# Performance work log

Measured on AMD Instinct MI355X. Metric: run time of the kernel, lower is better.

Reference implementation:

```python
import jax, jax.numpy as jnp
import numpy as np

NC, ND = 100000, 100000
E, L = 500000, 100000
HID, OUT = 128, 64
NH, HD = 4, 32
NL = 2


def setup_inputs() -> dict:
    key = jax.random.key(0)
    ks = jax.random.split(key, 16)
    f = jnp.float32
    s_lin = 1.0 / np.sqrt(HID)
    s_rel = 1.0 / np.sqrt(HD)
    return {
        "emb_C": jax.random.normal(ks[0], (NC, HID), f) * 0.1,
        "emb_D": jax.random.normal(ks[1], (ND, HID), f) * 0.1,
        "kW": jax.random.normal(ks[2], (NL, 2, HID, HID), f) * s_lin,
        "kb": jnp.zeros((NL, 2, HID), f),
        "qW": jax.random.normal(ks[3], (NL, 2, HID, HID), f) * s_lin,
        "qb": jnp.zeros((NL, 2, HID), f),
        "vW": jax.random.normal(ks[4], (NL, 2, HID, HID), f) * s_lin,
        "vb": jnp.zeros((NL, 2, HID), f),
        "aW": jax.random.normal(ks[5], (NL, 2, HID, HID), f) * s_lin,
        "ab": jnp.zeros((NL, 2, HID), f),
        "skip": jnp.ones((NL, 2), f),
        "arel": jax.random.normal(ks[6], (NL, 2, NH, HD, HD), f) * s_rel,
        "mrel": jax.random.normal(ks[7], (NL, 2, NH, HD, HD), f) * s_rel,
        "prel": jnp.ones((NL, 2, NH), f),
        "outW": jax.random.normal(ks[8], (2, HID, OUT), f) * s_lin,
        "outb": jnp.zeros((2, OUT), f),
        # edge_index for (Compound -> Disease) and reverse (Disease -> Compound)
        "ei_cd": jnp.stack([jax.random.randint(ks[9], (E,), 0, NC),
                            jax.random.randint(ks[10], (E,), 0, ND)]).astype(jnp.int32),
        "ei_dc": jnp.stack([jax.random.randint(ks[11], (E,), 0, ND),
                            jax.random.randint(ks[12], (E,), 0, NC)]).astype(jnp.int32),
        # edge_label_index: (Compound, Disease) pairs to score
        "eli": jnp.stack([jax.random.randint(ks[13], (L,), 0, NC),
                          jax.random.randint(ks[14], (L,), 0, ND)]).astype(jnp.int32),
    }


def _seg_softmax(a, seg, n):
    # numerically stable softmax over edges grouped by destination node
    amax = jax.ops.segment_max(a, seg, num_segments=n)
    amax = jnp.where(jnp.isfinite(amax), amax, 0.0)
    ex = jnp.exp(a - amax[seg])
    den = jax.ops.segment_sum(ex, seg, num_segments=n)
    return ex / (den[seg] + 1e-16)


def _hgt_layer(xs, p, ei_cd, ei_dc):
    kW, kb, qW, qb, vW, vb, aW, ab, skip, arel, mrel, prel = p
    # per-node-type K/Q/V projections, reshaped to [N, heads, head_dim]
    k = [(xs[t] @ kW[t] + kb[t]).reshape(-1, NH, HD) for t in range(2)]
    q = [(xs[t] @ qW[t] + qb[t]).reshape(-1, NH, HD) for t in range(2)]
    v = [(xs[t] @ vW[t] + vb[t]).reshape(-1, NH, HD) for t in range(2)]
    outs = [jnp.zeros_like(k[0]), jnp.zeros_like(k[1])]
    rels = [(0, 1, ei_cd), (1, 0, ei_dc)]  # (src_type, dst_type, edge_index)
    for r, (s, d, ei) in enumerate(rels):
        # relation-specific transforms applied per source node (as in PyG HGTConv)
        krel = jnp.einsum('nhd,hde->nhe', k[s], arel[r])
        vrel = jnp.einsum('nhd,hde->nhe', v[s], mrel[r])
        src, dst = ei[0], ei[1]
        ndst = xs[d].shape[0]
        a = (q[d][dst] * krel[src]).sum(-1) * prel[r] / np.sqrt(HD)  # [E, NH]
        alpha = _seg_softmax(a, dst, ndst)
        msg = vrel[src] * alpha[..., None]                           # [E, NH, HD]
        outs[d] = outs[d] + jax.ops.segment_sum(msg, dst, num_segments=ndst)
    new = []
    for t in range(2):
        o = outs[t].reshape(-1, HID)
        o = jax.nn.gelu(o) @ aW[t] + ab[t]
        g = jax.nn.sigmoid(skip[t])
        new.append(g * o + (1.0 - g) * xs[t])  # skip connection (in==out dims)
    return new


def reference(emb_C, emb_D, kW, kb, qW, qb, vW, vb, aW, ab, skip, arel, mrel, prel,
              outW, outb, ei_cd, ei_dc, eli):
    xs = [emb_C, emb_D]
    for l in range(NL):
        p = (kW[l], kb[l], qW[l], qb[l], vW[l], vb[l], aW[l], ab[l],
             skip[l], arel[l], mrel[l], prel[l])
        xs = _hgt_layer(xs, p, ei_cd, ei_dc)
        xs = [jax.nn.relu(x) for x in xs]  # dropout(0.2) in eval mode -> identity
    zC = xs[0] @ outW[0] + outb[0]
    zD = xs[1] @ outW[1] + outb[1]
    logits = jnp.clip((zC[eli[0]] * zD[eli[1]]).sum(-1), -10.0, 10.0)
    return logits
```

## Files before the change

kernel.cpp:

```cpp
#include <hip/hip_runtime.h>
#include <math.h>

#define NC_   100000
#define ND_   100000
#define NN_   100000
#define E_CNT 500000
#define L_CNT 100000
#define NH_   4
#define HD_   32
#define WCAT_SZ (129 * 384)

typedef __attribute__((ext_vector_type(8))) short short8;
typedef __attribute__((ext_vector_type(4))) float floatx4;

__device__ __forceinline__ float gelu_f(float x) {
    const float c0 = 0.7978845608028654f;
    float x3 = x * x * x;
    return 0.5f * x * (1.0f + tanhf(c0 * (x + 0.044715f * x3)));
}

__device__ __forceinline__ unsigned short bf_rne(float x) {
    unsigned int u = __float_as_uint(x);
    u += 0x7fffu + ((u >> 16) & 1u);
    return (unsigned short)(u >> 16);
}
__device__ __forceinline__ float bf_to_f(unsigned short b) {
    return __uint_as_float(((unsigned int)b) << 16);
}

__global__ __launch_bounds__(256) void fill0_int(int* __restrict__ p, int n) {
    int i = blockIdx.x * 256 + threadIdx.x;
    if (i < n) p[i] = 0;
}

__global__ __launch_bounds__(256) void count_dst(const int* __restrict__ dstA,
                                                 const int* __restrict__ dstB,
                                                 int* __restrict__ cnt) {
    int r = blockIdx.y;
    const int* dst = r ? dstB : dstA;
    int e = blockIdx.x * 256 + threadIdx.x;
    if (e < E_CNT) atomicAdd(&cnt[r * NN_ + dst[e]], 1);
}

__global__ __launch_bounds__(256) void scan_a(const int* __restrict__ cnt,
                                              int* __restrict__ excl,
                                              int* __restrict__ partials) {
    __shared__ int sd[256];
    int r = blockIdx.y;
    cnt += r * NN_; excl += r * (NN_ + 1); partials += r * 128;
    int b = blockIdx.x, t = threadIdx.x;
    int base = b * 1024 + t * 4;
    int v0 = (base + 0 < NN_) ? cnt[base + 0] : 0;
    int v1 = (base + 1 < NN_) ? cnt[base + 1] : 0;
    int v2 = (base + 2 < NN_) ? cnt[base + 2] : 0;
    int v3 = (base + 3 < NN_) ? cnt[base + 3] : 0;
    int tsum = v0 + v1 + v2 + v3;
    sd[t] = tsum; __syncthreads();
    for (int off = 1; off < 256; off <<= 1) {
        int x = (t >= off) ? sd[t - off] : 0;
        __syncthreads();
        sd[t] += x;
        __syncthreads();
    }
    int excl_t = sd[t] - tsum;
    if (t == 255) partials[b] = sd[t];
    int q = excl_t;
    if (base + 0 < NN_) excl[base + 0] = q; q += v0;
    if (base + 1 < NN_) excl[base + 1] = q; q += v1;
    if (base + 2 < NN_) excl[base + 2] = q; q += v2;
    if (base + 3 < NN_) excl[base + 3] = q;
}

__global__ __launch_bounds__(128) void scan_b(int* __restrict__ partials) {
    __shared__ int sd[128];
    partials += blockIdx.x * 128;
    int t = threadIdx.x;
    int orig = (t < 98) ? partials[t] : 0;
    sd[t] = orig; __syncthreads();
    for (int off = 1; off < 128; off <<= 1) {
        int x = (t >= off) ? sd[t - off] : 0;
        __syncthreads();
        sd[t] += x;
        __syncthreads();
    }
    if (t < 98) partials[t] = sd[t] - orig;
}

__global__ __launch_bounds__(256) void scan_c(int* __restrict__ row_ptr,
                                              const int* __restrict__ partials,
                                              int* __restrict__ cursor) {
    int r = blockIdx.y;
    row_ptr += r * (NN_ + 1); partials += r * 128; cursor += r * NN_;
    int b = blockIdx.x, t = threadIdx.x;
    int base = b * 1024 + t * 4;
    int add = partials[b];
    #pragma unroll
    for (int j = 0; j < 4; j++) {
        int i = base + j;
        if (i < NN_) { int v = row_ptr[i] + add; row_ptr[i] = v; cursor[i] = v; }
    }
    if (b == 0 && t == 0) row_ptr[NN_] = E_CNT;
}

__global__ __launch_bounds__(256) void scatter_edges(const int* __restrict__ srcA,
                                                     const int* __restrict__ dstA,
                                                     const int* __restrict__ srcB,
                                                     const int* __restrict__ dstB,
                                                     int* __restrict__ cursor,
                                                     int* __restrict__ srcs) {
    int r = blockIdx.y;
    const int* src = r ? srcB : srcA;
    const int* dst = r ? dstB : dstA;
    cursor += r * NN_; srcs += r * E_CNT;
    int e = blockIdx.x * 256 + threadIdx.x;
    if (e >= E_CNT) return;
    int pos = atomicAdd(&cursor[dst[e]], 1);
    srcs[pos] = src[e];
}

__global__ void fuse_weights(const float* __restrict__ qW, const float* __restrict__ qb,
                             const float* __restrict__ kW, const float* __restrict__ kb,
                             const float* __restrict__ vW, const float* __restrict__ vb,
                             const float* __restrict__ arel, const float* __restrict__ mrel,
                             float* __restrict__ WcatAll)
{
    int i  = blockIdx.x;
    int t  = blockIdx.y;
    int lyr = blockIdx.z;
    int oc = threadIdx.x;
    int lt = lyr * 2 + t;
    float* Wcat = WcatAll + (size_t)lt * WCAT_SZ;
    float val;
    if (oc < 128) {
        val = (i < 128) ? qW[(size_t)(lt * 128 + i) * 128 + oc] : qb[lt * 128 + oc];
    } else {
        int which = (oc >= 256);
        int cc = oc - (which ? 256 : 128);
        int h = cc >> 5, e = cc & 31;
        const float* W = which ? vW : kW;
        const float* b = which ? vb : kb;
        const float* R = (which ? mrel : arel) + (size_t)(lt * NH_ + h) * HD_ * HD_ + e;
        float s = 0.f;
        if (i < 128) {
            const float* wrow = W + (size_t)(lt * 128 + i) * 128 + h * 32;
            #pragma unroll
            for (int d2 = 0; d2 < 32; d2++) s += wrow[d2] * R[d2 * 32];
        } else {
            const float* brow = b + lt * 128 + h * 32;
            #pragma unroll
            for (int d2 = 0; d2 < 32; d2++) s += brow[d2] * R[d2 * 32];
        }
        val = s;
    }
    Wcat[(size_t)((i < 128) ? i : 128) * 384 + oc] = val;
}

__global__ __launch_bounds__(256)
void pack_w(const float* __restrict__ W, int ldw, int matStride,
            unsigned short* __restrict__ out, int N, int outMatStride)
{
    int mat = blockIdx.y;
    int e = blockIdx.x * 256 + threadIdx.x;
    int total = N * 16;
    if (e >= total) return;
    int lane = e & 63;
    int s = (e >> 6) & 3;
    int nt = e >> 8;
    int col = nt * 16 + (lane & 15);
    int k0 = s * 32 + ((lane >> 4) << 3);
    const float* src = W + (size_t)mat * matStride + (size_t)k0 * ldw + col;
    int ps = N * 128;
    unsigned short* o = out + (size_t)mat * outMatStride + (size_t)e * 8;
    short8 p0, p1, p2;
    #pragma unroll
    for (int j = 0; j < 8; j++) {
        float x = src[(size_t)j * ldw];
        unsigned short b0 = bf_rne(x);
        float x1 = x - bf_to_f(b0);
        unsigned short b1 = bf_rne(x1);
        float x2 = x1 - bf_to_f(b1);
        unsigned short b2 = bf_rne(x2);
        p0[j] = (short)b0; p1[j] = (short)b1; p2[j] = (short)b2;
    }
    *(short8*)(o)          = p0;
    *(short8*)(o + ps)     = p1;
    *(short8*)(o + 2 * ps) = p2;
}

template<int TN, int POST>
__global__ __launch_bounds__(256, 4)
void gemm_mfma(const float* __restrict__ A, int lda,
               const unsigned short* __restrict__ Bp, int pstride,
               const float* __restrict__ bias,
               float* __restrict__ C, int ldc, int M,
               const float* __restrict__ resid, const float* __restrict__ skipv,
               int ySplit,
               const float* __restrict__ A2, const unsigned short* __restrict__ Bp2,
               int pstride2, const float* __restrict__ bias2,
               float* __restrict__ C2, int ldc2)
{
    constexpr int CT = TN / 16;
    int by = blockIdx.y;
    if (ySplit >= 0 && by >= ySplit) {
        A = A2; Bp = Bp2; pstride = pstride2; bias = bias2; C = C2; ldc = ldc2;
        by -= ySplit;
    }
    int tid  = threadIdx.x;
    int wave = tid >> 6, lane = tid & 63;
    int quad = lane >> 4, l16 = lane & 15;
    int bm = blockIdx.x * 64;
    int bn = by * TN;

    int row = bm + wave * 16 + l16;
    bool rv = row < M;
    const float* ap = A + (size_t)row * lda + quad * 8;
    const unsigned short* bp = Bp + (size_t)(bn >> 4) * 2048 + (size_t)lane * 8;

    floatx4 acc[CT];
    #pragma unroll
    for (int ct = 0; ct < CT; ct++) acc[ct] = (floatx4){0.f, 0.f, 0.f, 0.f};

    for (int s = 0; s < 4; s++) {
        float xv[8];
        if (rv) {
            *(float4*)&xv[0] = *(const float4*)(ap + s * 32);
            *(float4*)&xv[4] = *(const float4*)(ap + s * 32 + 4);
        } else {
            #pragma unroll
            for (int i = 0; i < 8; i++) xv[i] = 0.f;
        }
        short8 af0, af1, af2;
        #pragma unroll
        for (int i = 0; i < 8; i++) {
            float x = xv[i];
            unsigned short b0 = bf_rne(x);
            float x1 = x - bf_to_f(b0);
            unsigned short b1 = bf_rne(x1);
            float x2 = x1 - bf_to_f(b1);
            unsigned short b2 = bf_rne(x2);
            af0[i] = (short)b0; af1[i] = (short)b1; af2[i] = (short)b2;
        }
        #pragma unroll
        for (int ct = 0; ct < CT; ct++) {
            const unsigned short* bf = bp + (size_t)ct * 2048 + s * 512;
            short8 b0 = *(const short8*)(bf);
            short8 b1 = *(const short8*)(bf + pstride);
            short8 b2 = *(const short8*)(bf + 2 * (size_t)pstride);
            acc[ct] = __builtin_amdgcn_mfma_f32_16x16x32_bf16(af0, b2, acc[ct], 0, 0, 0);
            acc[ct] = __builtin_amdgcn_mfma_f32_16x16x32_bf16(af1, b1, acc[ct], 0, 0, 0);
            acc[ct] = __builtin_amdgcn_mfma_f32_16x16x32_bf16(af2, b0, acc[ct], 0, 0, 0);
            acc[ct] = __builtin_amdgcn_mfma_f32_16x16x32_bf16(af0, b1, acc[ct], 0, 0, 0);
            acc[ct] = __builtin_amdgcn_mfma_f32_16x16x32_bf16(af1, b0, acc[ct], 0, 0, 0);
            acc[ct] = __builtin_amdgcn_mfma_f32_16x16x32_bf16(af0, b0, acc[ct], 0, 0, 0);
        }
    }

    float g = 0.f, omg = 0.f;
    if (POST) { float sv = skipv[0]; g = 1.0f / (1.0f + expf(-sv)); omg = 1.0f - g; }
    #pragma unroll
    for (int ct = 0; ct < CT; ct++) {
        int col = bn + ct * 16 + l16;
        float bv = bias[col];
        #pragma unroll
        for (int i = 0; i < 4; i++) {
            int r = bm + wave * 16 + quad * 4 + i;
            if (r < M) {
                float v = acc[ct][i] + bv;
                if (POST) {
                    float rr = resid[(size_t)r * ldc + col];
                    v = fmaxf(g * v + omg * rr, 0.f);
                }
                C[(size_t)r * ldc + col] = v;
            }
        }
    }
}

__global__ __launch_bounds__(256)
void attn_gather(const int* __restrict__ row_ptr, const int* __restrict__ srcs,
                 float* __restrict__ qo, const float* __restrict__ kv,
                 const float* __restrict__ prel, int ndst)
{
    int wave = (blockIdx.x * 256 + threadIdx.x) >> 6;
    int lane = threadIdx.x & 63;
    if (wave >= ndst) return;
    int d = wave;
    int gl = lane & 15;
    int group = lane >> 4;
    int h = gl >> 2;
    float pr = prel[h] * 0.17677669529663687f;
    int beg = row_ptr[d], end = row_ptr[d + 1];
    const float* qrow = qo + (size_t)d * 128 + gl * 8;
    float4 q0 = *(const float4*)(qrow);
    float4 q1 = *(const float4*)(qrow + 4);
    float m = -1.0e30f, l = 0.f;
    float4 acc0 = make_float4(0.f,0.f,0.f,0.f), acc1 = acc0;
    int nt = (end - beg + 3) >> 2;
    for (int t = 0; t < nt; t++) {
        int i = beg + (t << 2) + group;
        if (i < end) {
            int s = srcs[i];
            const float* row = kv + (size_t)s * 256 + gl * 8;
            float4 k0 = *(const float4*)(row);
            float4 k1 = *(const float4*)(row + 4);
            float4 v0 = *(const float4*)(row + 128);
            float4 v1 = *(const float4*)(row + 132);
            float part = q0.x*k0.x + q0.y*k0.y + q0.z*k0.z + q0.w*k0.w
                       + q1.x*k1.x + q1.y*k1.y + q1.z*k1.z + q1.w*k1.w;
            part += __shfl_xor(part, 1);
            part += __shfl_xor(part, 2);
            float a = part * pr;
            float mn = fmaxf(m, a);
            float scale = expf(m - mn);
            float p = expf(a - mn);
            l = l * scale + p;
            acc0.x = acc0.x * scale + p * v0.x;
            acc0.y = acc0.y * scale + p * v0.y;
            acc0.z = acc0.z * scale + p * v0.z;
            acc0.w = acc0.w * scale + p * v0.w;
            acc1.x = acc1.x * scale + p * v1.x;
            acc1.y = acc1.y * scale + p * v1.y;
            acc1.z = acc1.z * scale + p * v1.z;
            acc1.w = acc1.w * scale + p * v1.w;
            m = mn;
        }
    }
    #pragma unroll
    for (int mask = 16; mask <= 32; mask <<= 1) {
        float m_o = __shfl_xor(m, mask);
        float l_o = __shfl_xor(l, mask);
        float4 a0o, a1o;
        a0o.x = __shfl_xor(acc0.x, mask); a0o.y = __shfl_xor(acc0.y, mask);
        a0o.z = __shfl_xor(acc0.z, mask); a0o.w = __shfl_xor(acc0.w, mask);
        a1o.x = __shfl_xor(acc1.x, mask); a1o.y = __shfl_xor(acc1.y, mask);
        a1o.z = __shfl_xor(acc1.z, mask); a1o.w = __shfl_xor(acc1.w, mask);
        float mn = fmaxf(m, m_o);
        float s0 = expf(m - mn), s1 = expf(m_o - mn);
        l = l * s0 + l_o * s1;
        acc0.x = acc0.x * s0 + a0o.x * s1; acc0.y = acc0.y * s0 + a0o.y * s1;
        acc0.z = acc0.z * s0 + a0o.z * s1; acc0.w = acc0.w * s0 + a0o.w * s1;
        acc1.x = acc1.x * s0 + a1o.x * s1; acc1.y = acc1.y * s0 + a1o.y * s1;
        acc1.z = acc1.z * s0 + a1o.z * s1; acc1.w = acc1.w * s0 + a1o.w * s1;
        m = mn;
    }
    float inv = (beg == end) ? 0.f : 1.f / (l + 1e-16f);
    if (group == 0) {
        float* orow = qo + (size_t)d * 128 + gl * 8;
        float4 o0, o1;
        o0.x = gelu_f(acc0.x * inv); o0.y = gelu_f(acc0.y * inv);
        o0.z = gelu_f(acc0.z * inv); o0.w = gelu_f(acc0.w * inv);
        o1.x = gelu_f(acc1.x * inv); o1.y = gelu_f(acc1.y * inv);
        o1.z = gelu_f(acc1.z * inv); o1.w = gelu_f(acc1.w * inv);
        *(float4*)(orow)     = o0;
        *(float4*)(orow + 4) = o1;
    }
}

__global__ __launch_bounds__(256)
void score_pairs(const int* __restrict__ ic, const int* __restrict__ id,
                 const float* __restrict__ zC, const float* __restrict__ zD,
                 float* __restrict__ out)
{
    int gid = blockIdx.x * 256 + threadIdx.x;
    int p = gid >> 4, lane = gid & 15;
    if (p >= L_CNT) return;
    int c = ic[p], d = id[p];
    float4 a = *(const float4*)(zC + (size_t)c * 64 + lane * 4);
    float4 b = *(const float4*)(zD + (size_t)d * 64 + lane * 4);
    float s = a.x * b.x + a.y * b.y + a.z * b.z + a.w * b.w;
    s += __shfl_down(s, 8, 16);
    s += __shfl_down(s, 4, 16);
    s += __shfl_down(s, 2, 16);
    s += __shfl_down(s, 1, 16);
    if (lane == 0) out[p] = fminf(10.0f, fmaxf(-10.0f, s));
}

extern "C" void kernel_launch(void* const* d_in, const int* in_sizes, int n_in,
                              void* d_out, int out_size, void* d_ws, size_t ws_size,
                              hipStream_t stream)
{
    float* xC = (float*)d_in[0];
    float* xD = (float*)d_in[1];
    const float* kW   = (const float*)d_in[2];
    const float* kb   = (const float*)d_in[3];
    const float* qW   = (const float*)d_in[4];
    const float* qb   = (const float*)d_in[5];
    const float* vW   = (const float*)d_in[6];
    const float* vb   = (const float*)d_in[7];
    const float* aW   = (const float*)d_in[8];
    const float* ab   = (const float*)d_in[9];
    const float* skip = (const float*)d_in[10];
    const float* arel = (const float*)d_in[11];
    const float* mrel = (const float*)d_in[12];
    const float* prel = (const float*)d_in[13];
    const float* outW = (const float*)d_in[14];
    const float* outb = (const float*)d_in[15];
    const int* ei_cd  = (const int*)d_in[16];
    const int* ei_dc  = (const int*)d_in[17];
    const int* eli    = (const int*)d_in[18];

    float* ws = (float*)d_ws;
    size_t off = 0;
    float* kv    = ws + off; off += (size_t)NN_ * 256;
    float* qo    = ws + off; off += (size_t)NN_ * 128;
    float* Wcat  = ws + off; off += (size_t)4 * WCAT_SZ;
    unsigned short* WsCat = (unsigned short*)(ws + off); off += (4 * 3 * 384 * 128) / 2;
    unsigned short* aWs   = (unsigned short*)(ws + off); off += (4 * 3 * 128 * 128) / 2;
    unsigned short* outWs = (unsigned short*)(ws + off); off += (2 * 3 * 64 * 128) / 2;
    int* iws = (int*)(ws + off);
    size_t ioff = 0;
    int* rp      = iws + ioff; ioff += 2 * (NN_ + 1);
    int* srcsA   = iws + ioff; ioff += 2 * E_CNT;
    int* cnt     = iws + ioff; ioff += 2 * NN_;
    int* cursor  = iws + ioff; ioff += 2 * NN_;
    int* partial = iws + ioff; ioff += 256;
    float* zC = kv;
    float* zD = kv + (size_t)NN_ * 128;

    const int gridM = (NN_ + 63) / 64;
    const int gE    = (E_CNT + 255) / 256;
    const int gN2   = (2 * NN_ + 255) / 256;
    const int gScan = 98;
    const int gGath = (NN_ + 3) / 4;

    fill0_int<<<gN2, 256, 0, stream>>>(cnt, 2 * NN_);
    count_dst<<<dim3(gE, 2), 256, 0, stream>>>(ei_cd + E_CNT, ei_dc + E_CNT, cnt);
    scan_a<<<dim3(gScan, 2), 256, 0, stream>>>(cnt, rp, partial);
    scan_b<<<2, 128, 0, stream>>>(partial);
    scan_c<<<dim3(gScan, 2), 256, 0, stream>>>(rp, partial, cursor);
    scatter_edges<<<dim3(gE, 2), 256, 0, stream>>>(ei_cd, ei_cd + E_CNT,
                                                   ei_dc, ei_dc + E_CNT, cursor, srcsA);
    int* rp_cd   = rp;
    int* rp_dc   = rp + (NN_ + 1);
    int* srcs_cd = srcsA;
    int* srcs_dc = srcsA + E_CNT;

    fuse_weights<<<dim3(129, 2, 2), 384, 0, stream>>>(qW, qb, kW, kb, vW, vb,
                                                      arel, mrel, Wcat);
    pack_w<<<dim3((384 * 16 + 255) / 256, 4), 256, 0, stream>>>(
        Wcat, 384, WCAT_SZ, WsCat, 384, 3 * 384 * 128);
    pack_w<<<dim3((128 * 16 + 255) / 256, 4), 256, 0, stream>>>(
        aW, 128, 128 * 128, aWs, 128, 3 * 128 * 128);
    pack_w<<<dim3((64 * 16 + 255) / 256, 2), 256, 0, stream>>>(
        outW, 64, 128 * 64, outWs, 64, 3 * 64 * 128);

    const int PS_CAT = 384 * 128;
    const int PS_AW  = 128 * 128;
    const int PS_OW  = 64 * 128;

    for (int l = 0; l < 2; l++) {
        const float* abl = ab + (size_t)l * 2 * 128;
        float* WcC = Wcat + (size_t)(l * 2 + 0) * WCAT_SZ;
        float* WcD = Wcat + (size_t)(l * 2 + 1) * WCAT_SZ;
        const unsigned short* WsC = WsCat + (size_t)(l * 2 + 0) * 3 * PS_CAT;
        const unsigned short* WsD = WsCat + (size_t)(l * 2 + 1) * 3 * PS_CAT;
        const unsigned short* aWsD = aWs + (size_t)(l * 2 + 1) * 3 * PS_AW;
        const unsigned short* aWsC = aWs + (size_t)(l * 2 + 0) * 3 * PS_AW;

        gemm_mfma<128, 0><<<dim3(gridM, 3), 256, 0, stream>>>(
            xC, 128, WsC + 128 * 128, PS_CAT, WcC + 128 * 384 + 128, kv, 256, NC_,
            nullptr, nullptr,
            2, xD, WsD, PS_CAT, WcD + 128 * 384, qo, 128);
        attn_gather<<<gGath, 256, 0, stream>>>(rp_cd, srcs_cd, qo, kv,
                                               prel + (l * 2 + 0) * 4, ND_);

        gemm_mfma<128, 0><<<dim3(gridM, 2), 256, 0, stream>>>(
            xD, 128, WsD + 128 * 128, PS_CAT, WcD + 128 * 384 + 128, kv, 256, ND_,
            nullptr, nullptr, -1, nullptr, nullptr, 0, nullptr, nullptr, 0);

        gemm_mfma<128, 1><<<dim3(gridM, 1), 256, 0, stream>>>(
            qo, 128, aWsD, PS_AW, abl + 128, xD, 128, ND_,
            xD, skip + l * 2 + 1, -1, nullptr, nullptr, 0, nullptr, nullptr, 0);

        gemm_mfma<128, 0><<<dim3(gridM, 1), 256, 0, stream>>>(
            xC, 128, WsC, PS_CAT, WcC + 128 * 384, qo, 128, NC_,
            nullptr, nullptr, -1, nullptr, nullptr, 0, nullptr, nullptr, 0);
        attn_gather<<<gGath, 256, 0, stream>>>(rp_dc, srcs_dc, qo, kv,
                                               prel + (l * 2 + 1) * 4, NC_);

        gemm_mfma<128, 1><<<dim3(gridM, 1), 256, 0, stream>>>(
            qo, 128, aWsC, PS_AW, abl, xC, 128, NC_,
            xC, skip + l * 2 + 0, -1, nullptr, nullptr, 0, nullptr, nullptr, 0);
    }

    gemm_mfma<64, 0><<<dim3(gridM, 2), 256, 0, stream>>>(
        xC, 128, outWs, PS_OW, outb, zC, 64, NC_, nullptr, nullptr,
        1, xD, outWs + 3 * PS_OW, PS_OW, outb + 64, zD, 64);

    score_pairs<<<(L_CNT * 16 + 255) / 256, 256, 0, stream>>>(
        eli, eli + L_CNT, zC, zD, (float*)d_out);
}
```

Baseline: 1.301 ms.

## Retile MFMA GEMM into 32x64 per-wave register tiles for operand reuse

Restructures the split-bf16 MFMA GEMM so each wave computes a 32-row by 64-column tile: two A row-fragments share the preloaded B fragments, and for TN=128 waves are split into two column groups. Block row coverage changes with TN (64 rows for TN=128, 128 rows for TN=64), and the final output GEMM grid is halved to match. The aim is to cut redundant B loads and A split work per MFMA. In exchange it uses more registers, which is why launch bounds drop from 4 to 3 blocks per CU.

```diff
diff --git a/kernel.cpp b/kernel.cpp
--- a/kernel.cpp
+++ b/kernel.cpp
@@ -26,6 +26,18 @@
 }
 __device__ __forceinline__ float bf_to_f(unsigned short b) {
     return __uint_as_float(((unsigned int)b) << 16);
+}
+
+__device__ __forceinline__ void split3(const float* xv, short8* f) {
+    #pragma unroll
+    for (int i = 0; i < 8; i++) {
+        float x = xv[i];
+        unsigned short b0 = bf_rne(x);
+        float x1 = x - bf_to_f(b0);
+        unsigned short b1 = bf_rne(x1);
+        float x2 = x1 - bf_to_f(b1);
+        f[0][i] = (short)b0; f[1][i] = (short)b1; f[2][i] = (short)bf_rne(x2);
+    }
 }
 
 __global__ __launch_bounds__(256) void fill0_int(int* __restrict__ p, int n) {
@@ -188,7 +200,7 @@
 }
 
 template<int TN, int POST>
-__global__ __launch_bounds__(256, 4)
+__global__ __launch_bounds__(256, 3)
 void gemm_mfma(const float* __restrict__ A, int lda,
                const unsigned short* __restrict__ Bp, int pstride,
                const float* __restrict__ bias,
@@ -199,7 +211,9 @@
                int pstride2, const float* __restrict__ bias2,
                float* __restrict__ C2, int ldc2)
 {
-    constexpr int CT = TN / 16;
+    constexpr int WCOLS = (TN >= 128) ? 2 : 1;
+    constexpr int WROWS = 4 / WCOLS;
+    constexpr int BROWS = WROWS * 32;
     int by = blockIdx.y;
     if (ySplit >= 0 && by >= ySplit) {
         A = A2; Bp = Bp2; pstride = pstride2; bias = bias2; C = C2; ldc = ldc2;
@@ -208,69 +222,84 @@
     int tid  = threadIdx.x;
     int wave = tid >> 6, lane = tid & 63;
     int quad = lane >> 4, l16 = lane & 15;
-    int bm = blockIdx.x * 64;
-    int bn = by * TN;
-
-    int row = bm + wave * 16 + l16;
-    bool rv = row < M;
-    const float* ap = A + (size_t)row * lda + quad * 8;
+    int wc = wave % WCOLS, wr = wave / WCOLS;
+    int bm = blockIdx.x * BROWS;
+    int bn = by * TN + wc * 64;
+
+    int row0 = bm + wr * 32 + l16;
+    bool rv0 = row0 < M;
+    bool rv1 = (row0 + 16) < M;
+    const float* ap0 = A + (size_t)row0 * lda + quad * 8;
+    const float* ap1 = ap0 + (size_t)16 * lda;
     const unsigned short* bp = Bp + (size_t)(bn >> 4) * 2048 + (size_t)lane * 8;
 
-    floatx4 acc[CT];
+    floatx4 acc[2][4];
     #pragma unroll
-    for (int ct = 0; ct < CT; ct++) acc[ct] = (floatx4){0.f, 0.f, 0.f, 0.f};
+    for (int m = 0; m < 2; m++)
+        #pragma unroll
+        for (int ct = 0; ct < 4; ct++) acc[m][ct] = (floatx4){0.f, 0.f, 0.f, 0.f};
+
+    constexpr int PA[6] = {0, 1, 2, 0, 1, 0};
+    constexpr int PB[6] = {2, 1, 0, 1, 0, 0};
 
     for (int s = 0; s < 4; s++) {
-        float xv[8];
-        if (rv) {
-            *(float4*)&xv[0] = *(const float4*)(ap + s * 32);
-            *(float4*)&xv[4] = *(const float4*)(ap + s * 32 + 4);
+        float xv0[8], xv1[8];
+        if (rv0) {
+            *(float4*)&xv0[0] = *(const float4*)(ap0 + s * 32);
+            *(float4*)&xv0[4] = *(const float4*)(ap0 + s * 32 + 4);
         } else {
             #pragma unroll
-            for (int i = 0; i < 8; i++) xv[i] = 0.f;
-        }
-        short8 af0, af1, af2;
+            for (int i = 0; i < 8; i++) xv0[i] = 0.f;
+        }
+        if (rv1) {
+            *(float4*)&xv1[0] = *(const float4*)(ap1 + s * 32);
+            *(float4*)&xv1[4] = *(const float4*)(ap1 + s * 32 + 4);
+        } else {
+            #pragma unroll
+            for (int i = 0; i < 8; i++) xv1[i] = 0.f;
+        }
+        short8 bfr[4][3];
         #pragma unroll
-        for (int i = 0; i < 8; i++) {
-            float x = xv[i];
-            unsigned short b0 = bf_rne(x);
-            float x1 = x - bf_to_f(b0);
-            unsigned short b1 = bf_rne(x1);
-            float x2 = x1 - bf_to_f(b1);
-            unsigned short b2 = bf_rne(x2);
-            af0[i] = (short)b0; af1[i] = (short)b1; af2[i] = (short)b2;
-        }
+        for (int ct = 0; ct < 4; ct++) {
+            const unsigned short* bf = bp + ct * 2048 + s * 512;
+            #pragma unroll
+            for (int p = 0; p < 3; p++)
+                bfr[ct][p] = *(const short8*)(bf + (size_t)p * pstride);
+        }
+        short8 af0[3], af1[3];
+        split3(xv0, af0);
+        split3(xv1, af1);
         #pragma unroll
-        for (int ct = 0; ct < CT; ct++) {
-            const unsigned short* bf = bp + (size_t)ct * 2048 + s * 512;
-            short8 b0 = *(const short8*)(bf);
-            short8 b1 = *(const short8*)(bf + pstride);
-            short8 b2 = *(const short8*)(bf + 2 * (size_t)pstride);
-            acc[ct] = __builtin_amdgcn_mfma_f32_16x16x32_bf16(af0, b2, acc[ct], 0, 0, 0);
-            acc[ct] = __builtin_amdgcn_mfma_f32_16x16x32_bf16(af1, b1, acc[ct], 0, 0, 0);
-            acc[ct] = __builtin_amdgcn_mfma_f32_16x16x32_bf16(af2, b0, acc[ct], 0, 0, 0);
-            acc[ct] = __builtin_amdgcn_mfma_f32_16x16x32_bf16(af0, b1, acc[ct], 0, 0, 0);
-            acc[ct] = __builtin_amdgcn_mfma_f32_16x16x32_bf16(af1, b0, acc[ct], 0, 0, 0);
-            acc[ct] = __builtin_amdgcn_mfma_f32_16x16x32_bf16(af0, b0, acc[ct], 0, 0, 0);
+        for (int o = 0; o < 6; o++) {
+            #pragma unroll
+            for (int ct = 0; ct < 4; ct++) {
+                acc[0][ct] = __builtin_amdgcn_mfma_f32_16x16x32_bf16(
+                    af0[PA[o]], bfr[ct][PB[o]], acc[0][ct], 0, 0, 0);
+                acc[1][ct] = __builtin_amdgcn_mfma_f32_16x16x32_bf16(
+                    af1[PA[o]], bfr[ct][PB[o]], acc[1][ct], 0, 0, 0);
+            }
         }
     }
 
     float g = 0.f, omg = 0.f;
     if (POST) { float sv = skipv[0]; g = 1.0f / (1.0f + expf(-sv)); omg = 1.0f - g; }
     #pragma unroll
-    for (int ct = 0; ct < CT; ct++) {
-        int col = bn + ct * 16 + l16;
-        float bv = bias[col];
+    for (int m = 0; m < 2; m++) {
         #pragma unroll
-        for (int i = 0; i < 4; i++) {
-            int r = bm + wave * 16 + quad * 4 + i;
-            if (r < M) {
-                float v = acc[ct][i] + bv;
-                if (POST) {
-                    float rr = resid[(size_t)r * ldc + col];
-                    v = fmaxf(g * v + omg * rr, 0.f);
+        for (int ct = 0; ct < 4; ct++) {
+            int col = bn + ct * 16 + l16;
+            float bv = bias[col];
+            #pragma unroll
+            for (int i = 0; i < 4; i++) {
+                int r = bm + wr * 32 + m * 16 + quad * 4 + i;
+                if (r < M) {
+                    float v = acc[m][ct][i] + bv;
+                    if (POST) {
+                        float rr = resid[(size_t)r * ldc + col];
+                        v = fmaxf(g * v + omg * rr, 0.f);
+                    }
+                    C[(size_t)r * ldc + col] = v;
                 }
-                C[(size_t)r * ldc + col] = v;
             }
         }
     }
@@ -418,6 +447,7 @@
     float* zD = kv + (size_t)NN_ * 128;
 
     const int gridM = (NN_ + 63) / 64;
+    const int gridM2 = (NN_ + 127) / 128;
     const int gE    = (E_CNT + 255) / 256;
     const int gN2   = (2 * NN_ + 255) / 256;
     const int gScan = 98;
@@ -483,7 +513,7 @@
             xC, skip + l * 2 + 0, -1, nullptr, nullptr, 0, nullptr, nullptr, 0);
     }
 
-    gemm_mfma<64, 0><<<dim3(gridM, 2), 256, 0, stream>>>(
+    gemm_mfma<64, 0><<<dim3(gridM2, 2), 256, 0, stream>>>(
         xC, 128, outWs, PS_OW, outb, zC, 64, NC_, nullptr, nullptr,
         1, xD, outWs + 3 * PS_OW, PS_OW, outb + 64, zD, 64);
 
```

Result: faster. 1.265 ms (-2.8%).
